# Kernel tuning notes

Measured on AMD Instinct MI355X. Metric: run time of the kernel, lower is better.

Reference implementation:

```python
import jax, jax.numpy as jnp
import numpy as np

NEG_SLOPE = 0.2
HEADS = 8

def _gat_conv(x, src, dst, n_nodes, W, att_src, att_dst, bias):
    # x: [N, Fin], W: [Fin, H*C], att_*: [H, C], bias: [C]
    H, C = att_src.shape
    xl = (x @ W).reshape(n_nodes, H, C)                      # [N,H,C]
    a_src = (xl * att_src[None]).sum(-1)                      # [N,H]
    a_dst = (xl * att_dst[None]).sum(-1)                      # [N,H]
    e = jax.nn.leaky_relu(a_src[src] + a_dst[dst], NEG_SLOPE) # [E,H]
    m = jax.ops.segment_max(e, dst, num_segments=n_nodes)     # [N,H]
    ee = jnp.exp(e - m[dst])
    s = jax.ops.segment_sum(ee, dst, num_segments=n_nodes)    # [N,H]
    alpha = ee / s[dst]                                       # [E,H]
    msg = alpha[:, :, None] * xl[src]                         # [E,H,C]
    out = jax.ops.segment_sum(msg, dst, num_segments=n_nodes) # [N,H,C]
    return out.mean(axis=1) + bias                            # [N,C] (concat=False)

def setup_inputs() -> dict:
    key = jax.random.key(0)
    ks = jax.random.split(key, 12)
    N, E, EL = 50000, 800000, 200000
    V, D, HID, OUT = 5000, 128, 32, 32
    inp = {}
    inp['x'] = jax.random.randint(ks[0], (N,), 0, V)
    inp['edge_index'] = jax.random.randint(ks[1], (2, E), 0, N)
    inp['edge_label_index'] = jax.random.randint(ks[2], (2, EL), 0, N)
    inp['emb'] = jax.random.normal(ks[3], (V, D), jnp.float32) * D ** -0.5
    inp['W1'] = jax.random.normal(ks[4], (D, HEADS * HID), jnp.float32) * D ** -0.5
    inp['att_src1'] = jax.random.normal(ks[5], (HEADS, HID), jnp.float32) * HID ** -0.5
    inp['att_dst1'] = jax.random.normal(ks[6], (HEADS, HID), jnp.float32) * HID ** -0.5
    inp['b1'] = jnp.zeros((HID,), jnp.float32)
    inp['W2'] = jax.random.normal(ks[7], (HID, HEADS * OUT), jnp.float32) * HID ** -0.5
    inp['att_src2'] = jax.random.normal(ks[8], (HEADS, OUT), jnp.float32) * OUT ** -0.5
    inp['att_dst2'] = jax.random.normal(ks[9], (HEADS, OUT), jnp.float32) * OUT ** -0.5
    inp['b2'] = jnp.zeros((OUT,), jnp.float32)
    return inp

def reference(x, edge_index, edge_label_index, emb, W1, att_src1, att_dst1, b1, W2, att_src2, att_dst2, b2):
    N = x.shape[0]
    # PyG GATConv adds self-loops by default
    loop = jnp.arange(N)
    src = jnp.concatenate([edge_index[0], loop])
    dst = jnp.concatenate([edge_index[1], loop])
    h = emb[x]                                                   # [N, D] embedding lookup (squeeze(1) equivalent)
    h = jax.nn.relu(_gat_conv(h, src, dst, N, W1, att_src1, att_dst1, b1))
    # dropout p=0.5 is identity at inference (training=False)
    z = _gat_conv(h, src, dst, N, W2, att_src2, att_dst2, b2)    # [N, OUT]
    # decode: dot product over label edges
    return (z[edge_label_index[0]] * z[edge_label_index[1]]).sum(axis=-1)
```

## Files before the change

### kernel.cpp

```cpp
#include <hip/hip_runtime.h>
#include <hip/hip_fp16.h>
#include <math.h>
#include <limits.h>

#define HH 8
#define CC 32
#define NEG 0.2f

struct __align__(8) half4 { __half2 a, b; };

__device__ __forceinline__ int ldnt(const int* p){ return __builtin_nontemporal_load(p); }
__device__ __forceinline__ float ldntf(const float* p){ return __builtin_nontemporal_load(p); }

__device__ __forceinline__ void edge_sd_nt(const int* __restrict__ ei, int e, int E, int& s, int& d){
  if(e < E){ s = ldnt(ei+e); d = ldnt(ei+E+e); } else { s = e-E; d = s; }
}


__global__ void k_zero(int* __restrict__ p, int n){
  int i = blockIdx.x*blockDim.x + threadIdx.x;
  if(i < n) p[i] = 0;
}

__global__ void k_count(const int* __restrict__ ei, int E, int ET, int* __restrict__ cnt){
  int e = blockIdx.x*blockDim.x + threadIdx.x;
  if(e >= ET) return;
  int d = (e < E) ? ldnt(ei+E+e) : e-E;
  atomicAdd(&cnt[d], 1);
}

__global__ __launch_bounds__(256) void k_scan_block(const int* __restrict__ cnt,
                                                    int* __restrict__ off,
                                                    int* __restrict__ bsum, int N){
  int i = blockIdx.x*256 + threadIdx.x;
  int v = (i < N) ? cnt[i] : 0;
  int lane = threadIdx.x & 63;
  int incl = v;
  #pragma unroll
  for(int o=1;o<64;o<<=1){ int u = __shfl_up(incl,o); if(lane>=o) incl += u; }
  __shared__ int wsum[4];
  if(lane==63) wsum[threadIdx.x>>6] = incl;
  __syncthreads();
  int w = threadIdx.x>>6, wadd = 0;
  #pragma unroll
  for(int k=0;k<4;k++) if(k<w) wadd += wsum[k];
  if(i < N) off[i] = wadd + incl - v;
  if(threadIdx.x==255) bsum[blockIdx.x] = wadd + incl;
}

__global__ __launch_bounds__(256) void k_scan_bsum(int* __restrict__ bsum, int nb,
                                                   int* __restrict__ offN){
  int t = threadIdx.x;
  int v = (t < nb) ? bsum[t] : 0;
  int lane = t & 63;
  int incl = v;
  #pragma unroll
  for(int o=1;o<64;o<<=1){ int u = __shfl_up(incl,o); if(lane>=o) incl += u; }
  __shared__ int wsum[4];
  if(lane==63) wsum[t>>6] = incl;
  __syncthreads();
  int w = t>>6, wadd = 0;
  #pragma unroll
  for(int k=0;k<4;k++) if(k<w) wadd += wsum[k];
  if(t < nb) bsum[t] = wadd + incl - v;
  if(t == 255) *offN = wadd + incl;
}

__global__ void k_scan_add(int* __restrict__ off, const int* __restrict__ bsum,
                           int* __restrict__ cur, int N){
  int i = blockIdx.x*256 + threadIdx.x;
  if(i < N){ int v = off[i] + bsum[blockIdx.x]; off[i] = v; cur[i] = v; }
}

__global__ void k_scatter(const int* __restrict__ ei, int E, int ET,
                          const int* __restrict__ x,
                          int* __restrict__ cur, int* __restrict__ csr_src,
                          int* __restrict__ csr_xv){
  int e = blockIdx.x*blockDim.x + threadIdx.x;
  if(e >= ET) return;
  int s,d; edge_sd_nt(ei,e,E,s,d);
  int pos = atomicAdd(&cur[d], 1);
  csr_src[pos] = s;
  csr_xv[pos]  = x[s];
}

__global__ __launch_bounds__(256) void k_ws(const float* __restrict__ W2,
                                            const float* __restrict__ att_s2,
                                            const float* __restrict__ att_d2,
                                            float* __restrict__ ws_s, float* __restrict__ ws_d){
  int k = threadIdx.x >> 3, h = threadIdx.x & 7;
  float ss = 0.f, dd = 0.f;
  for(int c=0;c<CC;c++){
    float w = W2[k*256 + h*CC + c];
    ss = fmaf(w, att_s2[h*CC+c], ss);
    dd = fmaf(w, att_d2[h*CC+c], dd);
  }
  ws_s[k*HH+h] = ss;
  ws_d[k*HH+h] = dd;
}

__global__ __launch_bounds__(256,4) void k_gemm1(
    const float* __restrict__ X, const float* __restrict__ W,
    const float* __restrict__ att_s, const float* __restrict__ att_d,
    __half* __restrict__ xl, float* __restrict__ a_src, float* __restrict__ a_dst, int V){
  const int ROWS = 8, FIN = 128;
  __shared__ __align__(16) float xs[ROWS][FIN];
  int row0 = blockIdx.x*ROWS;
  int tid = threadIdx.x;
  for(int p = tid; p < ROWS*FIN; p += 256){
    int r = p/FIN, kk = p - r*FIN;
    int row = row0 + r;
    xs[r][kk] = (row < V) ? ldntf(X + (size_t)row*FIN + kk) : 0.f;
  }
  __syncthreads();
  float acc[ROWS];
  #pragma unroll
  for(int r=0;r<ROWS;r++) acc[r]=0.f;
  for(int k=0;k<FIN;k++){
    float w = W[(size_t)k*256 + tid];
    #pragma unroll
    for(int r=0;r<ROWS;r++) acc[r] = fmaf(xs[r][k], w, acc[r]);
  }
  float as = att_s[tid], ad = att_d[tid];
  #pragma unroll
  for(int r=0;r<ROWS;r++){
    int n = row0+r;
    float v = acc[r];
    float ps = v*as, pd = v*ad;
    #pragma unroll
    for(int msk=16; msk>=1; msk>>=1){
      ps += __shfl_xor(ps, msk);
      pd += __shfl_xor(pd, msk);
    }
    if(n < V){
      xl[(size_t)n*256 + tid] = __float2half(v);
      if((tid&31)==0){
        int hh = tid>>5;
        a_src[n*HH+hh] = ps;
        a_dst[n*HH+hh] = pd;
      }
    }
  }
}

__global__ __launch_bounds__(256) void k_fused1(
    const int* __restrict__ off, const int* __restrict__ csr_xv,
    const int* __restrict__ x,
    const float* __restrict__ a_src_v, const float* __restrict__ a_dst_v,
    const __half* __restrict__ xl_v, const float* __restrict__ bias,
    const float* __restrict__ ws_s, const float* __restrict__ ws_d,
    __half* __restrict__ h2h, float* __restrict__ a_src2, float* __restrict__ a_dst2, int N){
  int wid = (int)((blockIdx.x*(size_t)blockDim.x + threadIdx.x) >> 6);
  int lane = threadIdx.x & 63;
  if(wid >= N) return;
  const int start = off[wid], end = off[wid+1];
  const int t = lane >> 3, h = lane & 7;
  const int xv_n = x[wid];
  const float ad = a_dst_v[xv_n*HH + h];

  float m = -INFINITY;
  for(int j0 = start; j0 < end; j0 += 8){
    int jj = j0 + t;
    if(jj < end){
      float v = a_src_v[ldnt(csr_xv + jj)*HH + h] + ad;
      v = v > 0.f ? v : NEG*v;
      m = fmaxf(m, v);
    }
  }
  #pragma unroll
  for(int msk=8; msk<64; msk<<=1) m = fmaxf(m, __shfl_xor(m, msk));

  const int h2 = lane >> 3, c0 = (lane & 7)*4;
  const __half* xp = xl_v + h2*CC + c0;
  float eesum = 0.f;
  float4 acc = make_float4(0.f,0.f,0.f,0.f);
  for(int j0 = start; j0 < end; j0 += 8){
    int jj = j0 + t;
    int sv = 0;
    float ee = 0.f;
    if(jj < end){
      sv = ldnt(csr_xv + jj);
      float v = a_src_v[sv*HH + h] + ad;
      v = v > 0.f ? v : NEG*v;
      ee = expf(v - m);
      eesum += ee;
    }
    #pragma unroll
    for(int u=0; u<8; ++u){
      float a  = __shfl(ee, u*8 + h2);
      int   ss = __shfl(sv, u*8);
      half4 hv = *reinterpret_cast<const half4*>(xp + (size_t)ss*256);
      float2 f01 = __half22float2(hv.a), f23 = __half22float2(hv.b);
      acc.x = fmaf(a, f01.x, acc.x);
      acc.y = fmaf(a, f01.y, acc.y);
      acc.z = fmaf(a, f23.x, acc.z);
      acc.w = fmaf(a, f23.y, acc.w);
    }
  }
  #pragma unroll
  for(int msk=8; msk<64; msk<<=1) eesum += __shfl_xor(eesum, msk);
  float is2 = 0.125f / __shfl(eesum, h2);
  acc.x *= is2; acc.y *= is2; acc.z *= is2; acc.w *= is2;
  #pragma unroll
  for(int msk=8; msk<64; msk<<=1){
    acc.x += __shfl_xor(acc.x, msk);
    acc.y += __shfl_xor(acc.y, msk);
    acc.z += __shfl_xor(acc.z, msk);
    acc.w += __shfl_xor(acc.w, msk);
  }
  if(lane < 8){
    const float4 b = *reinterpret_cast<const float4*>(bias + c0);
    float4 o = make_float4(fmaxf(acc.x+b.x,0.f), fmaxf(acc.y+b.y,0.f),
                           fmaxf(acc.z+b.z,0.f), fmaxf(acc.w+b.w,0.f));
    half4 hv;
    hv.a = __floats2half2_rn(o.x, o.y);
    hv.b = __floats2half2_rn(o.z, o.w);
    *reinterpret_cast<half4*>(h2h + (size_t)wid*CC + c0) = hv;
    float ps = 0.f, pd = 0.f;
    #pragma unroll
    for(int g=0; g<8; ++g){
      float v0 = __shfl(o.x, g), v1 = __shfl(o.y, g), v2 = __shfl(o.z, g), v3 = __shfl(o.w, g);
      int kb = g*4;
      ps = fmaf(v0, ws_s[(kb+0)*HH+lane], ps);
      ps = fmaf(v1, ws_s[(kb+1)*HH+lane], ps);
      ps = fmaf(v2, ws_s[(kb+2)*HH+lane], ps);
      ps = fmaf(v3, ws_s[(kb+3)*HH+lane], ps);
      pd = fmaf(v0, ws_d[(kb+0)*HH+lane], pd);
      pd = fmaf(v1, ws_d[(kb+1)*HH+lane], pd);
      pd = fmaf(v2, ws_d[(kb+2)*HH+lane], pd);
      pd = fmaf(v3, ws_d[(kb+3)*HH+lane], pd);
    }
    a_src2[wid*HH + lane] = ps;
    a_dst2[wid*HH + lane] = pd;
  }
}

__global__ __launch_bounds__(256) void k_fused2(
    const int* __restrict__ off, const int* __restrict__ csr_src,
    const float* __restrict__ a_src2, const float* __restrict__ a_dst2,
    const __half* __restrict__ h2h, const float* __restrict__ W2,
    const float* __restrict__ b2, float* __restrict__ z, int N){
  __shared__ __align__(16) float aggl[4][256];
  int w = threadIdx.x >> 6;
  int wid = (int)(blockIdx.x*4 + w);
  int lane = threadIdx.x & 63;
  bool active = wid < N;
  int start = 0, end = 0;
  const int t = lane >> 3, h = lane & 7;
  float ad = 0.f;
  if(active){
    start = off[wid]; end = off[wid+1];
    ad = a_dst2[wid*HH + h];
  }

  float m = -INFINITY;
  for(int j0 = start; j0 < end; j0 += 8){
    int jj = j0 + t;
    if(jj < end){
      float v = a_src2[ldnt(csr_src + jj)*HH + h] + ad;
      v = v > 0.f ? v : NEG*v;
      m = fmaxf(m, v);
    }
  }
  #pragma unroll
  for(int msk=8; msk<64; msk<<=1) m = fmaxf(m, __shfl_xor(m, msk));

  const int h2 = lane >> 3, k0 = (lane & 7)*4;
  const __half* hp = h2h + k0;
  float eesum = 0.f;
  float4 acc = make_float4(0.f,0.f,0.f,0.f);
  for(int j0 = start; j0 < end; j0 += 8){
    int jj = j0 + t;
    int s = 0;
    float ee = 0.f;
    if(jj < end){
      s = ldnt(csr_src + jj);
      float v = a_src2[s*HH + h] + ad;
      v = v > 0.f ? v : NEG*v;
      ee = expf(v - m);
      eesum += ee;
    }
    #pragma unroll
    for(int u=0; u<8; ++u){
      float a  = __shfl(ee, u*8 + h2);
      int   ss = __shfl(s,  u*8);
      half4 hv = *reinterpret_cast<const half4*>(hp + (size_t)ss*CC);
      float2 f01 = __half22float2(hv.a), f23 = __half22float2(hv.b);
      acc.x = fmaf(a, f01.x, acc.x);
      acc.y = fmaf(a, f01.y, acc.y);
      acc.z = fmaf(a, f23.x, acc.z);
      acc.w = fmaf(a, f23.y, acc.w);
    }
  }
  #pragma unroll
  for(int msk=8; msk<64; msk<<=1) eesum += __shfl_xor(eesum, msk);
  float is2 = 0.125f / __shfl(eesum, h2);
  *reinterpret_cast<float4*>(&aggl[w][h2*CC + k0]) =
      make_float4(acc.x*is2, acc.y*is2, acc.z*is2, acc.w*is2);
  __syncthreads();

  const int ch = lane & 31, part = lane >> 5;
  float p = 0.f;
  #pragma unroll
  for(int hh = 0; hh < 4; ++hh){
    int hq = part*4 + hh;
    const float* wcol = W2 + hq*CC + ch;
    const float* arow = &aggl[w][hq*CC];
    #pragma unroll 8
    for(int k=0;k<CC;k++) p = fmaf(arow[k], wcol[(size_t)k*256], p);
  }
  p += __shfl_xor(p, 32);
  if(active && part==0) z[(size_t)wid*CC + ch] = p + b2[ch];
}

__global__ void k_decode(const int* __restrict__ eli, int EL,
                         const float* __restrict__ z, float* __restrict__ out){
  int e = blockIdx.x*blockDim.x + threadIdx.x;
  if(e >= EL) return;
  const float4* za = reinterpret_cast<const float4*>(z + (size_t)ldnt(eli+e)*CC);
  const float4* zb = reinterpret_cast<const float4*>(z + (size_t)ldnt(eli+EL+e)*CC);
  float s = 0.f;
  #pragma unroll
  for(int j=0;j<8;j++){
    float4 u = za[j], v = zb[j];
    s += u.x*v.x + u.y*v.y + u.z*v.z + u.w*v.w;
  }
  out[e] = s;
}

extern "C" void kernel_launch(void* const* d_in, const int* in_sizes, int n_in,
                              void* d_out, int out_size, void* d_ws, size_t ws_size,
                              hipStream_t stream){
  const int*   x   = (const int*)d_in[0];
  const int*   ei  = (const int*)d_in[1];
  const int*   eli = (const int*)d_in[2];
  const float* emb = (const float*)d_in[3];
  const float* W1  = (const float*)d_in[4];
  const float* as1 = (const float*)d_in[5];
  const float* ad1 = (const float*)d_in[6];
  const float* b1  = (const float*)d_in[7];
  const float* W2  = (const float*)d_in[8];
  const float* as2 = (const float*)d_in[9];
  const float* ad2 = (const float*)d_in[10];
  const float* b2  = (const float*)d_in[11];

  const int N  = in_sizes[0];
  const int V  = in_sizes[3]/128;
  const int E  = in_sizes[1]/2;
  const int EL = in_sizes[2]/2;
  const int ET = E + N;

  __half* xl_v = (__half*)d_ws;
  __half* h2h  = xl_v + (size_t)V*256;
  float* a_src_v = (float*)(h2h + (size_t)N*CC);
  float* a_dst_v = a_src_v + (size_t)V*HH;
  float* a_src2  = a_dst_v + (size_t)V*HH;
  float* a_dst2  = a_src2 + (size_t)N*HH;
  float* z       = a_dst2 + (size_t)N*HH;
  float* ws_s    = z + (size_t)N*CC;
  float* ws_d    = ws_s + 256;
  int*   cnt   = (int*)(ws_d + 256);
  int*   off   = cnt + N;
  int*   cur   = off + N + 1;
  int*   bsum  = cur + N;
  int*   csr   = bsum + ((N+255)/256);
  int*   csr_xv= csr + ET;

  dim3 blk(256);
  auto cdiv = [](long long a, long long b){ return (unsigned)((a+b-1)/b); };
  const int nb = (int)cdiv(N,256);

  k_zero<<<cdiv(N,256), blk, 0, stream>>>(cnt, N);
  k_count<<<cdiv(ET,256), blk, 0, stream>>>(ei, E, ET, cnt);
  k_scan_block<<<nb, blk, 0, stream>>>(cnt, off, bsum, N);
  k_scan_bsum<<<1, blk, 0, stream>>>(bsum, nb, off + N);
  k_scan_add<<<nb, blk, 0, stream>>>(off, bsum, cur, N);
  k_scatter<<<cdiv(ET,256), blk, 0, stream>>>(ei, E, ET, x, cur, csr, csr_xv);

  k_ws<<<1, blk, 0, stream>>>(W2, as2, ad2, ws_s, ws_d);

  k_gemm1<<<cdiv(V,8), blk, 0, stream>>>(emb, W1, as1, ad1, xl_v, a_src_v, a_dst_v, V);
  k_fused1<<<cdiv((long long)N*64,256), blk, 0, stream>>>(off, csr_xv, x, a_src_v, a_dst_v,
                                                          xl_v, b1, ws_s, ws_d,
                                                          h2h, a_src2, a_dst2, N);

  k_fused2<<<cdiv((long long)N*64,256), blk, 0, stream>>>(off, csr, a_src2, a_dst2,
                                                          h2h, W2, b2, z, N);

  k_decode<<<cdiv(EL,256), blk, 0, stream>>>(eli, EL, z, (float*)d_out);
}
```

Measured before the change: 350.6 us.

## Replace per-node softmax max pass with global per-head upper bound

Removes the first pass over each node's incoming edges that computed the exact segment max. A small reduction kernel now computes the global max of a_src per head, and each node uses leaky_relu(gmax + a_dst) as its softmax shift. Because leaky_relu is monotone, this is an upper bound on every incoming logit, so the result is mathematically unchanged and only one gather pass over the edges remains. The risk is underflow in exp when the bound sits far above a node's true max, though with these logit magnitudes that gap stays small.

```diff
diff --git a/kernel.cpp b/kernel.cpp
--- a/kernel.cpp
+++ b/kernel.cpp
@@ -11,15 +11,17 @@
 
 __device__ __forceinline__ int ldnt(const int* p){ return __builtin_nontemporal_load(p); }
 __device__ __forceinline__ float ldntf(const float* p){ return __builtin_nontemporal_load(p); }
+__device__ __forceinline__ int f2ord(float f){ int i=__float_as_int(f); return i>=0? i : i^0x7fffffff; }
+__device__ __forceinline__ float ord2f(int i){ return __int_as_float(i>=0? i : i^0x7fffffff); }
 
 __device__ __forceinline__ void edge_sd_nt(const int* __restrict__ ei, int e, int E, int& s, int& d){
   if(e < E){ s = ldnt(ei+e); d = ldnt(ei+E+e); } else { s = e-E; d = s; }
 }
 
 
-__global__ void k_zero(int* __restrict__ p, int n){
+__global__ void k_seti(int* __restrict__ p, int n, int v){
   int i = blockIdx.x*blockDim.x + threadIdx.x;
-  if(i < n) p[i] = 0;
+  if(i < n) p[i] = v;
 }
 
 __global__ void k_count(const int* __restrict__ ei, int E, int ET, int* __restrict__ cnt){
@@ -97,6 +99,17 @@
   }
   ws_s[k*HH+h] = ss;
   ws_d[k*HH+h] = dd;
+}
+
+__global__ __launch_bounds__(256) void k_gmax(const float* __restrict__ a, int n8,
+                                              int* __restrict__ gmax){
+  int tid = blockIdx.x*256 + threadIdx.x;
+  int lane = threadIdx.x & 63;
+  float m = -INFINITY;
+  for(int i = tid; i < n8; i += gridDim.x*256) m = fmaxf(m, a[i]);
+  #pragma unroll
+  for(int msk=8; msk<64; msk<<=1) m = fmaxf(m, __shfl_xor(m, msk));
+  if(lane < 8) atomicMax(&gmax[lane], f2ord(m));
 }
 
 __global__ __launch_bounds__(256,4) void k_gemm1(
@@ -147,6 +160,7 @@
     const int* __restrict__ off, const int* __restrict__ csr_xv,
     const int* __restrict__ x,
     const float* __restrict__ a_src_v, const float* __restrict__ a_dst_v,
+    const int* __restrict__ gmax1,
     const __half* __restrict__ xl_v, const float* __restrict__ bias,
     const float* __restrict__ ws_s, const float* __restrict__ ws_d,
     __half* __restrict__ h2h, float* __restrict__ a_src2, float* __restrict__ a_dst2, int N){
@@ -157,18 +171,8 @@
   const int t = lane >> 3, h = lane & 7;
   const int xv_n = x[wid];
   const float ad = a_dst_v[xv_n*HH + h];
-
-  float m = -INFINITY;
-  for(int j0 = start; j0 < end; j0 += 8){
-    int jj = j0 + t;
-    if(jj < end){
-      float v = a_src_v[ldnt(csr_xv + jj)*HH + h] + ad;
-      v = v > 0.f ? v : NEG*v;
-      m = fmaxf(m, v);
-    }
-  }
-  #pragma unroll
-  for(int msk=8; msk<64; msk<<=1) m = fmaxf(m, __shfl_xor(m, msk));
+  float mb = ord2f(gmax1[h]) + ad;
+  mb = mb > 0.f ? mb : NEG*mb;
 
   const int h2 = lane >> 3, c0 = (lane & 7)*4;
   const __half* xp = xl_v + h2*CC + c0;
@@ -182,7 +186,7 @@
       sv = ldnt(csr_xv + jj);
       float v = a_src_v[sv*HH + h] + ad;
       v = v > 0.f ? v : NEG*v;
-      ee = expf(v - m);
+      ee = expf(v - mb);
       eesum += ee;
     }
     #pragma unroll
@@ -238,6 +242,7 @@
 __global__ __launch_bounds__(256) void k_fused2(
     const int* __restrict__ off, const int* __restrict__ csr_src,
     const float* __restrict__ a_src2, const float* __restrict__ a_dst2,
+    const int* __restrict__ gmax2,
     const __half* __restrict__ h2h, const float* __restrict__ W2,
     const float* __restrict__ b2, float* __restrict__ z, int N){
   __shared__ __align__(16) float aggl[4][256];
@@ -252,18 +257,8 @@
     start = off[wid]; end = off[wid+1];
     ad = a_dst2[wid*HH + h];
   }
-
-  float m = -INFINITY;
-  for(int j0 = start; j0 < end; j0 += 8){
-    int jj = j0 + t;
-    if(jj < end){
-      float v = a_src2[ldnt(csr_src + jj)*HH + h] + ad;
-      v = v > 0.f ? v : NEG*v;
-      m = fmaxf(m, v);
-    }
-  }
-  #pragma unroll
-  for(int msk=8; msk<64; msk<<=1) m = fmaxf(m, __shfl_xor(m, msk));
+  float mb = ord2f(gmax2[h]) + ad;
+  mb = mb > 0.f ? mb : NEG*mb;
 
   const int h2 = lane >> 3, k0 = (lane & 7)*4;
   const __half* hp = h2h + k0;
@@ -277,7 +272,7 @@
       s = ldnt(csr_src + jj);
       float v = a_src2[s*HH + h] + ad;
       v = v > 0.f ? v : NEG*v;
-      ee = expf(v - m);
+      ee = expf(v - mb);
       eesum += ee;
     }
     #pragma unroll
@@ -359,7 +354,9 @@
   float* z       = a_dst2 + (size_t)N*HH;
   float* ws_s    = z + (size_t)N*CC;
   float* ws_d    = ws_s + 256;
-  int*   cnt   = (int*)(ws_d + 256);
+  int*   gmax1   = (int*)(ws_d + 256);
+  int*   gmax2   = gmax1 + 8;
+  int*   cnt   = gmax2 + 8;
   int*   off   = cnt + N;
   int*   cur   = off + N + 1;
   int*   bsum  = cur + N;
@@ -370,7 +367,8 @@
   auto cdiv = [](long long a, long long b){ return (unsigned)((a+b-1)/b); };
   const int nb = (int)cdiv(N,256);
 
-  k_zero<<<cdiv(N,256), blk, 0, stream>>>(cnt, N);
+  k_seti<<<cdiv(N,256), blk, 0, stream>>>(cnt, N, 0);
+  k_seti<<<1, blk, 0, stream>>>(gmax1, 16, INT_MIN);
   k_count<<<cdiv(ET,256), blk, 0, stream>>>(ei, E, ET, cnt);
   k_scan_block<<<nb, blk, 0, stream>>>(cnt, off, bsum, N);
   k_scan_bsum<<<1, blk, 0, stream>>>(bsum, nb, off + N);
@@ -380,12 +378,14 @@
   k_ws<<<1, blk, 0, stream>>>(W2, as2, ad2, ws_s, ws_d);
 
   k_gemm1<<<cdiv(V,8), blk, 0, stream>>>(emb, W1, as1, ad1, xl_v, a_src_v, a_dst_v, V);
+  k_gmax<<<64, blk, 0, stream>>>(a_src_v, V*HH, gmax1);
   k_fused1<<<cdiv((long long)N*64,256), blk, 0, stream>>>(off, csr_xv, x, a_src_v, a_dst_v,
-                                                          xl_v, b1, ws_s, ws_d,
+                                                          gmax1, xl_v, b1, ws_s, ws_d,
                                                           h2h, a_src2, a_dst2, N);
 
+  k_gmax<<<64, blk, 0, stream>>>(a_src2, N*HH, gmax2);
   k_fused2<<<cdiv((long long)N*64,256), blk, 0, stream>>>(off, csr, a_src2, a_dst2,
-                                                          h2h, W2, b2, z, N);
+                                                          gmax2, h2h, W2, b2, z, N);
 
   k_decode<<<cdiv(EL,256), blk, 0, stream>>>(eli, EL, z, (float*)d_out);
 }
```

New measurement: 323.7 us. 7.7% less time.
